# Optimization experiments

Measured on AMD Instinct MI355X. Metric: run time of the kernel, lower is better.

## Reference

```python
import jax, jax.numpy as jnp
import numpy as np

NEG_SLOPE = 0.2  # PyG GATConv default leaky_relu negative_slope
BN_EPS = 1e-5


def gat_layer(x, src, dst, W, a_src, a_dst, bias):
    """PyG-style GATConv (self-loops already appended to src/dst).
    x: [N, F_in], W: [F_in, H*C], a_src/a_dst: [H, C], bias: [H*C].
    Returns [N, H*C] (concat heads)."""
    N = x.shape[0]
    H, C = a_src.shape
    h = (x @ W).reshape(N, H, C)                      # [N, H, C]
    al_src = jnp.sum(h * a_src[None], axis=-1)        # [N, H]
    al_dst = jnp.sum(h * a_dst[None], axis=-1)        # [N, H]
    e = jax.nn.leaky_relu(al_src[src] + al_dst[dst], NEG_SLOPE)  # [E, H]
    # segment softmax over destination neighborhoods
    m = jax.ops.segment_max(e, dst, num_segments=N)   # [N, H]
    ee = jnp.exp(e - m[dst])
    denom = jax.ops.segment_sum(ee, dst, num_segments=N)  # [N, H]
    alpha = ee / denom[dst]                           # [E, H]
    out = jax.ops.segment_sum(alpha[:, :, None] * h[src], dst, num_segments=N)  # [N, H, C]
    return out.reshape(N, H * C) + bias


def batch_norm(x, gamma, beta):
    mu = jnp.mean(x, axis=0)
    var = jnp.var(x, axis=0)  # biased, matches torch BN training stats
    return gamma * (x - mu) * jax.lax.rsqrt(var + BN_EPS) + beta


def setup_inputs() -> dict:
    key = jax.random.key(0)
    N, F, H, C = 50000, 128, 4, 64
    E = 400000
    HC = H * C  # 256
    ks = jax.random.split(key, 24)

    def glorot(k, shape, fan_in):
        return jax.random.normal(k, shape, dtype=jnp.float32) * (1.0 / np.sqrt(fan_in))

    inp = {
        "x": jax.random.normal(ks[0], (N, F), dtype=jnp.float32),
        "edge_index": jax.random.randint(ks[1], (2, E), 0, N, dtype=jnp.int64),
        # conv1: F -> H*C
        "W1": glorot(ks[2], (F, HC), F),
        "a1s": glorot(ks[3], (H, C), C),
        "a1d": glorot(ks[4], (H, C), C),
        "b1": jnp.zeros((HC,), jnp.float32),
        # conv2: H*C -> H*C
        "W2": glorot(ks[5], (HC, HC), HC),
        "a2s": glorot(ks[6], (H, C), C),
        "a2d": glorot(ks[7], (H, C), C),
        "b2": jnp.zeros((HC,), jnp.float32),
        # conv3: H*C -> C (1 head)
        "W3": glorot(ks[8], (HC, C), HC),
        "a3s": glorot(ks[9], (1, C), C),
        "a3d": glorot(ks[10], (1, C), C),
        "b3": jnp.zeros((C,), jnp.float32),
        # batch norms
        "g1": jnp.ones((HC,), jnp.float32),
        "be1": jnp.zeros((HC,), jnp.float32),
        "g2": jnp.ones((HC,), jnp.float32),
        "be2": jnp.zeros((HC,), jnp.float32),
        # MLP head: C -> C//2 -> 2
        "fw1": glorot(ks[11], (C, C // 2), C),
        "fb1": jnp.zeros((C // 2,), jnp.float32),
        "fw2": glorot(ks[12], (C // 2, 2), C // 2),
        "fb2": jnp.zeros((2,), jnp.float32),
    }
    return inp


def reference(x, edge_index, W1, a1s, a1d, b1, W2, a2s, a2d, b2,
              W3, a3s, a3d, b3, g1, be1, g2, be2, fw1, fb1, fw2, fb2):
    N = x.shape[0]
    loop = jnp.arange(N, dtype=edge_index.dtype)
    src = jnp.concatenate([edge_index[0], loop])  # self-loops (PyG default)
    dst = jnp.concatenate([edge_index[1], loop])

    h = gat_layer(x, src, dst, W1, a1s, a1d, b1)
    h = jax.nn.elu(batch_norm(h, g1, be1))
    h = gat_layer(h, src, dst, W2, a2s, a2d, b2)
    h = jax.nn.elu(batch_norm(h, g2, be2))
    h = jax.nn.elu(gat_layer(h, src, dst, W3, a3s, a3d, b3))
    h = jax.nn.relu(h @ fw1 + fb1)
    return h @ fw2 + fb2  # [N, 2] logits
```

## Files before the change

### kernel.cpp

```cpp
#include <hip/hip_runtime.h>
#include <math.h>
#include <stdint.h>

typedef __attribute__((ext_vector_type(8))) short short8v;
typedef __attribute__((ext_vector_type(4))) float float4v;

__device__ __forceinline__ float bf2f(unsigned short u) {
  return __uint_as_float((unsigned int)u << 16);
}
__device__ __forceinline__ unsigned short f2bf(float f) {
  unsigned int u = __float_as_uint(f);
  unsigned int r = (u + 0x7FFFu + ((u >> 16) & 1u)) >> 16;
  return (unsigned short)r;
}
__device__ __forceinline__ float exp_lrelu(float x) {
  x = x > 0.f ? x : 0.2f * x;
  return expf(x);
}

typedef __attribute__((address_space(3))) void lds_void;
typedef const __attribute__((address_space(1))) void glb_void;
__device__ __forceinline__ void gload_lds16(const void* g, void* l) {
  __builtin_amdgcn_global_load_lds((glb_void*)g, (lds_void*)l, 16, 0, 0);
}

__global__ void wprep_kernel(const float* __restrict__ W, unsigned short* __restrict__ Wh,
                             int K, int Nw)
{
  int t = blockIdx.x * 256 + threadIdx.x;
  if (t >= K * Nw) return;
  int i = t & 7;
  int lane = (t >> 3) & 63;
  int frag = t >> 9;
  int ktiles = K >> 5;
  int n_tile = frag / ktiles, k_tile = frag - n_tile * ktiles;
  int k = k_tile * 32 + ((lane >> 4) << 3) + i;
  int n = (n_tile << 4) + (lane & 15);
  Wh[t] = f2bf(W[(size_t)k * Nw + n]);
}

__global__ __launch_bounds__(256) void split_kernel(const float* __restrict__ in,
    unsigned short* __restrict__ hi, size_t n4)
{
  size_t i0 = (size_t)blockIdx.x * 256 + threadIdx.x;
  size_t stride = (size_t)gridDim.x * 256;
  for (size_t idx = i0; idx < n4; idx += stride) {
    float4 v = ((const float4*)in)[idx];
    ushort4 h;
    h.x = f2bf(v.x); h.y = f2bf(v.y); h.z = f2bf(v.z); h.w = f2bf(v.w);
    ((ushort4*)hi)[idx] = h;
  }
}

__global__ __launch_bounds__(256) void bnsplit_kernel(const unsigned short* __restrict__ act,
    const float* __restrict__ scale, const float* __restrict__ shift,
    unsigned short* __restrict__ hi, size_t nchunks)
{
  size_t i0 = (size_t)blockIdx.x * 256 + threadIdx.x;
  size_t stride = (size_t)gridDim.x * 256;
  for (size_t idx = i0; idx < nchunks; idx += stride) {
    ushort4 u = ((const ushort4*)act)[idx];
    int f = (int)((idx * 4) & 255);
    float4 sc = *(const float4*)(scale + f);
    float4 sh = *(const float4*)(shift + f);
    float v0 = fmaf(bf2f(u.x), sc.x, sh.x);
    float v1 = fmaf(bf2f(u.y), sc.y, sh.y);
    float v2 = fmaf(bf2f(u.z), sc.z, sh.z);
    float v3 = fmaf(bf2f(u.w), sc.w, sh.w);
    v0 = v0 > 0.f ? v0 : expm1f(v0);
    v1 = v1 > 0.f ? v1 : expm1f(v1);
    v2 = v2 > 0.f ? v2 : expm1f(v2);
    v3 = v3 > 0.f ? v3 : expm1f(v3);
    ushort4 h;
    h.x = f2bf(v0); h.y = f2bf(v1); h.z = f2bf(v2); h.w = f2bf(v3);
    ((ushort4*)hi)[idx] = h;
  }
}

template<int MI, int WM, int WN, int KSTEPS, int HEADS>
__global__ __launch_bounds__(256) void gemm_al(
    const unsigned short* __restrict__ Ah, const unsigned short* __restrict__ Bh,
    const float* __restrict__ a_s, const float* __restrict__ a_d,
    unsigned short* __restrict__ C, float* __restrict__ al_s, float* __restrict__ al_d,
    int M)
{
  constexpr int BM = WM * MI * 16;
  constexpr int NG = BM / 64;
  constexpr int TILEB = NG * 8192;
  constexpr int Nw = WN * 64, K = KSTEPS * 64;
  constexpr int KT32 = KSTEPS * 2;
  __shared__ __align__(16) unsigned char smem[2][TILEB];

  const int wid = threadIdx.x >> 6, lane = threadIdx.x & 63;
  const int wm = wid / WN, wn = wid % WN;
  const int m0 = blockIdx.x * BM;
  const int n0 = wn * 64;
  const int ar = lane & 15;
  const int cchunk = lane >> 4;
  const int ntile0 = n0 >> 4;

  float4v acc[MI][4];
#pragma unroll
  for (int mi = 0; mi < MI; ++mi)
#pragma unroll
    for (int ni = 0; ni < 4; ++ni)
      acc[mi][ni] = (float4v){0.f, 0.f, 0.f, 0.f};

  auto stage = [&](int buf, int ks) {
#pragma unroll
    for (int j = wid; j < NG * 8; j += 4) {
      int g = j >> 3, c = j & 7;
      const unsigned short* gp = Ah + (size_t)(m0 + g * 64 + lane) * K + ks * 64 + c * 8;
      gload_lds16(gp, &smem[buf][g * 8192 + c * 1024 + lane * 16]);
    }
  };

  stage(0, 0);
  int cur = 0;
  for (int ks = 0; ks < KSTEPS; ++ks) {
    __syncthreads();
    short8v bh[2][4];
#pragma unroll
    for (int hh = 0; hh < 2; ++hh)
#pragma unroll
      for (int ni = 0; ni < 4; ++ni) {
        int kt = ks * 2 + hh;
        size_t off = (((size_t)(ntile0 + ni) * KT32 + kt) * 64 + lane) * 8;
        bh[hh][ni] = *(const short8v*)(Bh + off);
      }
    if (ks + 1 < KSTEPS) stage(cur ^ 1, ks + 1);
    short8v ah[2][MI];
#pragma unroll
    for (int hh = 0; hh < 2; ++hh)
#pragma unroll
      for (int mi = 0; mi < MI; ++mi) {
        int row = wm * MI * 16 + mi * 16 + ar;
        int c = hh * 4 + cchunk;
        int off = (row >> 6) * 8192 + c * 1024 + (row & 63) * 16;
        ah[hh][mi] = *(const short8v*)&smem[cur][off];
      }
#pragma unroll
    for (int hh = 0; hh < 2; ++hh)
#pragma unroll
      for (int mi = 0; mi < MI; ++mi)
#pragma unroll
        for (int ni = 0; ni < 4; ++ni)
          acc[mi][ni] = __builtin_amdgcn_mfma_f32_16x16x32_bf16(ah[hh][mi], bh[hh][ni], acc[mi][ni], 0, 0, 0);
    cur ^= 1;
  }

  const int cc = lane & 15;
#pragma unroll
  for (int mi = 0; mi < MI; ++mi) {
    int rowb = m0 + wm * MI * 16 + mi * 16 + ((lane >> 4) << 2);
#pragma unroll
    for (int r = 0; r < 4; ++r) {
      int row = rowb + r;
      if (row < M) {
#pragma unroll
        for (int ni = 0; ni < 4; ++ni)
          C[(size_t)row * Nw + n0 + ni * 16 + cc] = f2bf(acc[mi][ni][r]);
      }
    }
  }

  const int head = (HEADS == 4) ? wn : 0;
  float as_[4], ad_[4];
#pragma unroll
  for (int ni = 0; ni < 4; ++ni) {
    as_[ni] = a_s[head * 64 + ni * 16 + cc];
    ad_[ni] = a_d[head * 64 + ni * 16 + cc];
  }
#pragma unroll
  for (int mi = 0; mi < MI; ++mi) {
#pragma unroll
    for (int r = 0; r < 4; ++r) {
      float h0 = bf2f(f2bf(acc[mi][0][r]));
      float h1 = bf2f(f2bf(acc[mi][1][r]));
      float h2 = bf2f(f2bf(acc[mi][2][r]));
      float h3 = bf2f(f2bf(acc[mi][3][r]));
      float ps = h0 * as_[0] + h1 * as_[1] + h2 * as_[2] + h3 * as_[3];
      float pd = h0 * ad_[0] + h1 * ad_[1] + h2 * ad_[2] + h3 * ad_[3];
#pragma unroll
      for (int off = 1; off < 16; off <<= 1) {
        ps += __shfl_xor(ps, off);
        pd += __shfl_xor(pd, off);
      }
      int row = m0 + wm * MI * 16 + mi * 16 + ((lane >> 4) << 2) + r;
      if (cc == 0 && row < M) {
        al_s[row * HEADS + head] = ps;
        al_d[row * HEADS + head] = pd;
      }
    }
  }
}

__global__ void count_kernel(const int* __restrict__ dst, int E, int Etot, int* __restrict__ counts)
{
  int e = blockIdx.x * 256 + threadIdx.x;
  if (e >= Etot) return;
  int d = (e < E) ? dst[e] : (e - E);
  atomicAdd(&counts[d], 1);
}

__global__ void block_sum_kernel(const int* __restrict__ counts, int N, int* __restrict__ bsums)
{
  __shared__ int sd[256];
  int i = blockIdx.x * 256 + threadIdx.x;
  sd[threadIdx.x] = (i < N) ? counts[i] : 0;
  __syncthreads();
  for (int off = 128; off; off >>= 1) {
    if (threadIdx.x < off) sd[threadIdx.x] += sd[threadIdx.x + off];
    __syncthreads();
  }
  if (threadIdx.x == 0) bsums[blockIdx.x] = sd[0];
}

__global__ void scan_bsums_kernel(int* bsums, int nb)
{
  __shared__ int sd[256];
  int t = threadIdx.x;
  int v = (t < nb) ? bsums[t] : 0;
  sd[t] = v;
  __syncthreads();
  for (int off = 1; off < 256; off <<= 1) {
    int x = (t >= off) ? sd[t - off] : 0;
    __syncthreads();
    sd[t] += x;
    __syncthreads();
  }
  if (t < nb) bsums[t] = sd[t] - v;
}

__global__ void scan_write_kernel(const int* __restrict__ counts, int N,
                                  const int* __restrict__ bsums, int* __restrict__ rowStart, int Etot)
{
  __shared__ int sd[256];
  int i = blockIdx.x * 256 + threadIdx.x;
  int v = (i < N) ? counts[i] : 0;
  sd[threadIdx.x] = v;
  __syncthreads();
  for (int off = 1; off < 256; off <<= 1) {
    int x = (threadIdx.x >= off) ? sd[threadIdx.x - off] : 0;
    __syncthreads();
    sd[threadIdx.x] += x;
    __syncthreads();
  }
  if (i < N) rowStart[i] = bsums[blockIdx.x] + sd[threadIdx.x] - v;
  if (i == N - 1) rowStart[N] = Etot;
}

__global__ void fill_kernel(const int* __restrict__ src, const int* __restrict__ dst,
                            int E, int Etot, const int* __restrict__ rowStart,
                            int* __restrict__ cursor, int* __restrict__ csrSrc)
{
  int e = blockIdx.x * 256 + threadIdx.x;
  if (e >= Etot) return;
  int s, d;
  if (e < E) { s = src[e]; d = dst[e]; } else { s = d = e - E; }
  int pos = rowStart[d] + atomicAdd(&cursor[d], 1);
  csrSrc[pos] = s;
}

template<int HC_, bool OUT16>
__global__ __launch_bounds__(256) void aggregate_fused(
    const unsigned short* __restrict__ h16,
    const float* __restrict__ als, const float* __restrict__ ald,
    const int* __restrict__ csrSrc, const int* __restrict__ rowStart,
    void* __restrict__ outp, int N, const float* __restrict__ bias, int doElu)
{
  constexpr int H_ = HC_ / 64;
  constexpr int FPL = HC_ / 64;
  __shared__ float ldsW[4][64 * H_];
  const int wl = threadIdx.x >> 6;
  int wid = blockIdx.x * 4 + wl;
  if (wid >= N) return;
  const int lane = threadIdx.x & 63;
  const int head = (H_ == 4) ? (lane >> 4) : 0;
  const int start = rowStart[wid], end = rowStart[wid + 1];

  float ad0, ad1, ad2, ad3;
  if (H_ == 4) {
    float4 adv = ((const float4*)ald)[wid];
    ad0 = adv.x; ad1 = adv.y; ad2 = adv.z; ad3 = adv.w;
  } else {
    ad0 = ald[wid]; ad1 = ad2 = ad3 = 0.f;
  }

  float acc[FPL] = {};
  float wsum = 0.f;

  for (int base = start; base < end; base += 64) {
    int cnt = end - base; if (cnt > 64) cnt = 64;
    int s_l = 0;
    if (lane < cnt) {
      s_l = csrSrc[base + lane];
      if (H_ == 4) {
        float4 av = ((const float4*)als)[s_l];
        float4 w4;
        w4.x = exp_lrelu(av.x + ad0);
        w4.y = exp_lrelu(av.y + ad1);
        w4.z = exp_lrelu(av.z + ad2);
        w4.w = exp_lrelu(av.w + ad3);
        *(float4*)&ldsW[wl][lane * 4] = w4;
      } else {
        ldsW[wl][lane] = exp_lrelu(als[s_l] + ad0);
      }
    }
    int i = 0;
    for (; i + 4 <= cnt; i += 4) {
      int s0 = __shfl(s_l, i);
      int s1 = __shfl(s_l, i + 1);
      int s2 = __shfl(s_l, i + 2);
      int s3 = __shfl(s_l, i + 3);
      float w0 = ldsW[wl][(i + 0) * H_ + head];
      float w1 = ldsW[wl][(i + 1) * H_ + head];
      float w2 = ldsW[wl][(i + 2) * H_ + head];
      float w3 = ldsW[wl][(i + 3) * H_ + head];
      if (FPL == 4) {
        ushort4 r0 = ((const ushort4*)(h16 + (size_t)s0 * HC_))[lane];
        ushort4 r1 = ((const ushort4*)(h16 + (size_t)s1 * HC_))[lane];
        ushort4 r2 = ((const ushort4*)(h16 + (size_t)s2 * HC_))[lane];
        ushort4 r3 = ((const ushort4*)(h16 + (size_t)s3 * HC_))[lane];
        wsum += (w0 + w1) + (w2 + w3);
        acc[0] = fmaf(w0, bf2f(r0.x), acc[0]);
        acc[1] = fmaf(w0, bf2f(r0.y), acc[1]);
        acc[2] = fmaf(w0, bf2f(r0.z), acc[2]);
        acc[3] = fmaf(w0, bf2f(r0.w), acc[3]);
        acc[0] = fmaf(w1, bf2f(r1.x), acc[0]);
        acc[1] = fmaf(w1, bf2f(r1.y), acc[1]);
        acc[2] = fmaf(w1, bf2f(r1.z), acc[2]);
        acc[3] = fmaf(w1, bf2f(r1.w), acc[3]);
        acc[0] = fmaf(w2, bf2f(r2.x), acc[0]);
        acc[1] = fmaf(w2, bf2f(r2.y), acc[1]);
        acc[2] = fmaf(w2, bf2f(r2.z), acc[2]);
        acc[3] = fmaf(w2, bf2f(r2.w), acc[3]);
        acc[0] = fmaf(w3, bf2f(r3.x), acc[0]);
        acc[1] = fmaf(w3, bf2f(r3.y), acc[1]);
        acc[2] = fmaf(w3, bf2f(r3.z), acc[2]);
        acc[3] = fmaf(w3, bf2f(r3.w), acc[3]);
      } else {
        unsigned short r0 = h16[(size_t)s0 * HC_ + lane];
        unsigned short r1 = h16[(size_t)s1 * HC_ + lane];
        unsigned short r2 = h16[(size_t)s2 * HC_ + lane];
        unsigned short r3 = h16[(size_t)s3 * HC_ + lane];
        wsum += (w0 + w1) + (w2 + w3);
        acc[0] = fmaf(w0, bf2f(r0), acc[0]);
        acc[0] = fmaf(w1, bf2f(r1), acc[0]);
        acc[0] = fmaf(w2, bf2f(r2), acc[0]);
        acc[0] = fmaf(w3, bf2f(r3), acc[0]);
      }
    }
    for (; i < cnt; ++i) {
      int s0 = __shfl(s_l, i);
      float w0 = ldsW[wl][i * H_ + head];
      wsum += w0;
      if (FPL == 4) {
        ushort4 r0 = ((const ushort4*)(h16 + (size_t)s0 * HC_))[lane];
        acc[0] = fmaf(w0, bf2f(r0.x), acc[0]);
        acc[1] = fmaf(w0, bf2f(r0.y), acc[1]);
        acc[2] = fmaf(w0, bf2f(r0.z), acc[2]);
        acc[3] = fmaf(w0, bf2f(r0.w), acc[3]);
      } else {
        unsigned short r0 = h16[(size_t)s0 * HC_ + lane];
        acc[0] = fmaf(w0, bf2f(r0), acc[0]);
      }
    }
  }

  float inv = 1.0f / wsum;
  if (FPL == 4) {
    float o0 = acc[0] * inv, o1 = acc[1] * inv, o2 = acc[2] * inv, o3 = acc[3] * inv;
    if (bias) {
      const float4 b = ((const float4*)bias)[lane];
      o0 += b.x; o1 += b.y; o2 += b.z; o3 += b.w;
    }
    if (doElu) {
      o0 = o0 > 0.f ? o0 : expm1f(o0);
      o1 = o1 > 0.f ? o1 : expm1f(o1);
      o2 = o2 > 0.f ? o2 : expm1f(o2);
      o3 = o3 > 0.f ? o3 : expm1f(o3);
    }
    if (OUT16) {
      ushort4 o;
      o.x = f2bf(o0); o.y = f2bf(o1); o.z = f2bf(o2); o.w = f2bf(o3);
      ((ushort4*)((unsigned short*)outp + (size_t)wid * HC_))[lane] = o;
    } else {
      ((float4*)((float*)outp + (size_t)wid * HC_))[lane] = make_float4(o0, o1, o2, o3);
    }
  } else {
    float o = acc[0] * inv;
    if (bias) o += bias[lane];
    if (doElu) o = o > 0.f ? o : expm1f(o);
    if (OUT16) ((unsigned short*)outp)[(size_t)wid * HC_ + lane] = f2bf(o);
    else       ((float*)outp)[(size_t)wid * HC_ + lane] = o;
  }
}

__global__ __launch_bounds__(256) void bn_stats_kernel(const unsigned short* __restrict__ x, int N,
                                float* __restrict__ partials)
{
  const int wid = threadIdx.x >> 6, lane = threadIdx.x & 63;
  const int gw = blockIdx.x * 4 + wid;
  const int tw = gridDim.x * 4;
  float4 s = make_float4(0.f, 0.f, 0.f, 0.f);
  float4 q = make_float4(0.f, 0.f, 0.f, 0.f);
#pragma unroll 4
  for (int r = gw; r < N; r += tw) {
    ushort4 u = ((const ushort4*)(x + (size_t)r * 256))[lane];
    float v0 = bf2f(u.x), v1 = bf2f(u.y), v2 = bf2f(u.z), v3 = bf2f(u.w);
    s.x += v0; s.y += v1; s.z += v2; s.w += v3;
    q.x = fmaf(v0, v0, q.x); q.y = fmaf(v1, v1, q.y);
    q.z = fmaf(v2, v2, q.z); q.w = fmaf(v3, v3, q.w);
  }
  __shared__ float ls[4][512];
  *(float4*)&ls[wid][lane * 4] = s;
  *(float4*)&ls[wid][256 + lane * 4] = q;
  __syncthreads();
  const int t = threadIdx.x;
  float a = ls[0][t] + ls[1][t] + ls[2][t] + ls[3][t];
  float b = ls[0][t + 256] + ls[1][t + 256] + ls[2][t + 256] + ls[3][t + 256];
  partials[blockIdx.x * 512 + t] = a;
  partials[blockIdx.x * 512 + 256 + t] = b;
}

__global__ void bn_final_kernel(const float* __restrict__ partials, int nblk,
                                const float* __restrict__ g, const float* __restrict__ be,
                                int N, float* __restrict__ scale, float* __restrict__ shift)
{
  int f = threadIdx.x;
  float s = 0.f, q = 0.f;
#pragma unroll 8
  for (int b = 0; b < nblk; ++b) {
    s += partials[b * 512 + f];
    q += partials[b * 512 + 256 + f];
  }
  float mu = s / N;
  float var = q / N - mu * mu;
  float rs = rsqrtf(var + 1e-5f);
  float sc = g[f] * rs;
  scale[f] = sc;
  shift[f] = be[f] - mu * sc;
}

__global__ __launch_bounds__(256) void mlp_kernel(const float* __restrict__ h,
                           const float* __restrict__ fw1,
                           const float* __restrict__ fb1, const float* __restrict__ fw2,
                           const float* __restrict__ fb2, float* __restrict__ out, int N)
{
  __shared__ float w1s[64][32];
  __shared__ float w2s[32][2];
  __shared__ float b1s[32];
  const int t = threadIdx.x;
  for (int i = t; i < 64 * 32; i += 256) w1s[i >> 5][i & 31] = fw1[i];
  if (t < 64) w2s[t >> 1][t & 1] = fw2[t];
  if (t < 32) b1s[t] = fb1[t];
  __syncthreads();

  int n = blockIdx.x * 256 + t;
  if (n >= N) return;

  float hv[64];
#pragma unroll
  for (int k4 = 0; k4 < 16; ++k4) {
    float4 v = *(const float4*)(h + (size_t)n * 64 + k4 * 4);
    hv[k4 * 4 + 0] = v.x; hv[k4 * 4 + 1] = v.y;
    hv[k4 * 4 + 2] = v.z; hv[k4 * 4 + 3] = v.w;
  }
  float hid[32];
#pragma unroll
  for (int j = 0; j < 32; ++j) hid[j] = b1s[j];
#pragma unroll
  for (int k = 0; k < 64; ++k) {
    float hk = hv[k];
#pragma unroll
    for (int jb = 0; jb < 8; ++jb) {
      float4 wv = *(const float4*)&w1s[k][jb * 4];
      hid[jb * 4 + 0] = fmaf(hk, wv.x, hid[jb * 4 + 0]);
      hid[jb * 4 + 1] = fmaf(hk, wv.y, hid[jb * 4 + 1]);
      hid[jb * 4 + 2] = fmaf(hk, wv.z, hid[jb * 4 + 2]);
      hid[jb * 4 + 3] = fmaf(hk, wv.w, hid[jb * 4 + 3]);
    }
  }
  float p0 = fb2[0], p1 = fb2[1];
#pragma unroll
  for (int j = 0; j < 32; ++j) {
    float r = fmaxf(hid[j], 0.f);
    p0 = fmaf(r, w2s[j][0], p0);
    p1 = fmaf(r, w2s[j][1], p1);
  }
  *(float2*)(out + (size_t)n * 2) = make_float2(p0, p1);
}

extern "C" void kernel_launch(void* const* d_in, const int* in_sizes, int n_in,
                              void* d_out, int out_size, void* d_ws, size_t ws_size,
                              hipStream_t stream)
{
  const float* x   = (const float*)d_in[0];
  const int*   ei  = (const int*)d_in[1];
  const float* W1  = (const float*)d_in[2];
  const float* a1s = (const float*)d_in[3];
  const float* a1d = (const float*)d_in[4];
  const float* W2  = (const float*)d_in[6];
  const float* a2s = (const float*)d_in[7];
  const float* a2d = (const float*)d_in[8];
  const float* W3  = (const float*)d_in[10];
  const float* a3s = (const float*)d_in[11];
  const float* a3d = (const float*)d_in[12];
  const float* b3  = (const float*)d_in[13];
  const float* g1  = (const float*)d_in[14];
  const float* be1 = (const float*)d_in[15];
  const float* g2  = (const float*)d_in[16];
  const float* be2 = (const float*)d_in[17];
  const float* fw1 = (const float*)d_in[18];
  const float* fb1 = (const float*)d_in[19];
  const float* fw2 = (const float*)d_in[20];
  const float* fb2 = (const float*)d_in[21];
  float* out = (float*)d_out;

  const int F = 128;
  const int N = in_sizes[0] / F;
  const int E = in_sizes[1] / 2;
  const int Etot = E + N;
  const int* srcIdx = ei;
  const int* dstIdx = ei + E;

  char* w = (char*)d_ws;
  auto alloc = [&](size_t bytes) -> void* {
    void* p = (void*)w;
    w += (bytes + 255) & ~(size_t)255;
    return p;
  };
  unsigned short* h16  = (unsigned short*)alloc((size_t)N * 256 * 2);
  unsigned short* act16= (unsigned short*)alloc((size_t)N * 256 * 2);
  float* actf    = (float*)alloc((size_t)N * 64 * 4);
  unsigned short* aBf  = (unsigned short*)alloc((size_t)N * 256 * 2);
  float* als     = (float*)alloc((size_t)N * 4 * 4);
  float* ald     = (float*)alloc((size_t)N * 4 * 4);
  int*   counts  = (int*)alloc((size_t)N * 4);
  int*   cursor  = (int*)alloc((size_t)N * 4);
  int*   rowStart= (int*)alloc((size_t)(N + 1) * 4);
  int*   csrSrc  = (int*)alloc((size_t)Etot * 4);
  int*   bsums   = (int*)alloc((size_t)((N + 255) / 256) * 4);
  float* partials= (float*)alloc((size_t)128 * 512 * 4);
  float* scale1  = (float*)alloc(256 * 4);
  float* shift1  = (float*)alloc(256 * 4);
  float* scale2  = (float*)alloc(256 * 4);
  float* shift2  = (float*)alloc(256 * 4);
  unsigned short* w1h = (unsigned short*)alloc((size_t)128 * 256 * 2);
  unsigned short* w2h = (unsigned short*)alloc((size_t)256 * 256 * 2);
  unsigned short* w3h = (unsigned short*)alloc((size_t)256 * 64 * 2);
  (void)alloc(65536);

  const int nb = (N + 255) / 256;
  const int ebk = (Etot + 255) / 256;
  const int aggBlocks = (N + 3) / 4;

  wprep_kernel<<<(128 * 256 + 255) / 256, 256, 0, stream>>>(W1, w1h, 128, 256);
  wprep_kernel<<<(256 * 256 + 255) / 256, 256, 0, stream>>>(W2, w2h, 256, 256);
  wprep_kernel<<<(256 * 64 + 255) / 256, 256, 0, stream>>>(W3, w3h, 256, 64);

  hipMemsetAsync(counts, 0, (size_t)N * 4, stream);
  hipMemsetAsync(cursor, 0, (size_t)N * 4, stream);
  count_kernel<<<ebk, 256, 0, stream>>>(dstIdx, E, Etot, counts);
  block_sum_kernel<<<nb, 256, 0, stream>>>(counts, N, bsums);
  scan_bsums_kernel<<<1, 256, 0, stream>>>(bsums, nb);
  scan_write_kernel<<<nb, 256, 0, stream>>>(counts, N, bsums, rowStart, Etot);
  fill_kernel<<<ebk, 256, 0, stream>>>(srcIdx, dstIdx, E, Etot, rowStart, cursor, csrSrc);

  dim3 g12((N + 63) / 64, 1);
  dim3 g3((N + 127) / 128, 1);

  split_kernel<<<2048, 256, 0, stream>>>(x, aBf, (size_t)N * 128 / 4);
  gemm_al<4, 1, 4, 2, 4><<<g12, 256, 0, stream>>>(aBf, w1h, a1s, a1d, h16, als, ald, N);
  aggregate_fused<256, true><<<aggBlocks, 256, 0, stream>>>(h16, als, ald, csrSrc, rowStart, act16, N, nullptr, 0);
  bn_stats_kernel<<<128, 256, 0, stream>>>(act16, N, partials);
  bn_final_kernel<<<1, 256, 0, stream>>>(partials, 128, g1, be1, N, scale1, shift1);

  bnsplit_kernel<<<2048, 256, 0, stream>>>(act16, scale1, shift1, aBf, (size_t)N * 64);
  gemm_al<4, 1, 4, 4, 4><<<g12, 256, 0, stream>>>(aBf, w2h, a2s, a2d, h16, als, ald, N);
  aggregate_fused<256, true><<<aggBlocks, 256, 0, stream>>>(h16, als, ald, csrSrc, rowStart, act16, N, nullptr, 0);
  bn_stats_kernel<<<128, 256, 0, stream>>>(act16, N, partials);
  bn_final_kernel<<<1, 256, 0, stream>>>(partials, 128, g2, be2, N, scale2, shift2);

  bnsplit_kernel<<<2048, 256, 0, stream>>>(act16, scale2, shift2, aBf, (size_t)N * 64);
  gemm_al<2, 4, 1, 4, 1><<<g3, 256, 0, stream>>>(aBf, w3h, a3s, a3d, h16, als, ald, N);
  aggregate_fused<64, false><<<aggBlocks, 256, 0, stream>>>(h16, als, ald, csrSrc, rowStart, actf, N, b3, 1);

  mlp_kernel<<<(N + 255) / 256, 256, 0, stream>>>(actf, fw1, fb1, fw2, fb2, out, N);
}
```

Baseline: 306.5 us.

## Split GEMM across 2D grid with 128-thread blocks, merge weight prep and memsets

The attention-fused GEMM now uses 128-thread blocks and a second grid dimension over column groups, so each block handles a 64-row tile and half the heads (or a smaller tile for the single-head layer). This roughly doubles the number of blocks and halves LDS per block, aiming for better occupancy and load balance. The A tile is then staged once per column-group block, so A traffic through L2 doubles. The three weight-conversion launches are merged into one kernel, and the two counter memsets into one contiguous memset, to cut launch overhead.

```diff
diff --git a/kernel.cpp b/kernel.cpp
--- a/kernel.cpp
+++ b/kernel.cpp
@@ -24,11 +24,9 @@
   __builtin_amdgcn_global_load_lds((glb_void*)g, (lds_void*)l, 16, 0, 0);
 }
 
-__global__ void wprep_kernel(const float* __restrict__ W, unsigned short* __restrict__ Wh,
-                             int K, int Nw)
-{
-  int t = blockIdx.x * 256 + threadIdx.x;
-  if (t >= K * Nw) return;
+__device__ __forceinline__ void wprep_one(const float* W, unsigned short* Wh,
+                                          int t, int K, int Nw)
+{
   int i = t & 7;
   int lane = (t >> 3) & 63;
   int frag = t >> 9;
@@ -37,6 +35,19 @@
   int k = k_tile * 32 + ((lane >> 4) << 3) + i;
   int n = (n_tile << 4) + (lane & 15);
   Wh[t] = f2bf(W[(size_t)k * Nw + n]);
+}
+
+__global__ void wprep_all_kernel(const float* __restrict__ W1, unsigned short* __restrict__ w1h,
+                                 const float* __restrict__ W2, unsigned short* __restrict__ w2h,
+                                 const float* __restrict__ W3, unsigned short* __restrict__ w3h)
+{
+  int t = blockIdx.x * 256 + threadIdx.x;
+  const int s1 = 128 * 256, s2 = 256 * 256, s3 = 256 * 64;
+  if (t < s1) { wprep_one(W1, w1h, t, 128, 256); return; }
+  t -= s1;
+  if (t < s2) { wprep_one(W2, w2h, t, 256, 256); return; }
+  t -= s2;
+  if (t < s3) { wprep_one(W3, w3h, t, 256, 64); }
 }
 
 __global__ __launch_bounds__(256) void split_kernel(const float* __restrict__ in,
@@ -78,23 +89,25 @@
 }
 
 template<int MI, int WM, int WN, int KSTEPS, int HEADS>
-__global__ __launch_bounds__(256) void gemm_al(
+__global__ __launch_bounds__(128) void gemm_al(
     const unsigned short* __restrict__ Ah, const unsigned short* __restrict__ Bh,
     const float* __restrict__ a_s, const float* __restrict__ a_d,
     unsigned short* __restrict__ C, float* __restrict__ al_s, float* __restrict__ al_d,
     int M)
 {
+  constexpr int NWAVES = WM * WN;
   constexpr int BM = WM * MI * 16;
-  constexpr int NG = BM / 64;
-  constexpr int TILEB = NG * 8192;
-  constexpr int Nw = WN * 64, K = KSTEPS * 64;
+  constexpr int TILEB = BM * 64 * 2;
+  constexpr int Nw = HEADS * 64;
+  constexpr int K = KSTEPS * 64;
   constexpr int KT32 = KSTEPS * 2;
   __shared__ __align__(16) unsigned char smem[2][TILEB];
 
   const int wid = threadIdx.x >> 6, lane = threadIdx.x & 63;
   const int wm = wid / WN, wn = wid % WN;
+  const int gn = blockIdx.y * WN + wn;
   const int m0 = blockIdx.x * BM;
-  const int n0 = wn * 64;
+  const int n0 = gn * 64;
   const int ar = lane & 15;
   const int cchunk = lane >> 4;
   const int ntile0 = n0 >> 4;
@@ -108,10 +121,9 @@
 
   auto stage = [&](int buf, int ks) {
 #pragma unroll
-    for (int j = wid; j < NG * 8; j += 4) {
-      int g = j >> 3, c = j & 7;
-      const unsigned short* gp = Ah + (size_t)(m0 + g * 64 + lane) * K + ks * 64 + c * 8;
-      gload_lds16(gp, &smem[buf][g * 8192 + c * 1024 + lane * 16]);
+    for (int c = wid; c < 8; c += NWAVES) {
+      const unsigned short* gp = Ah + (size_t)(m0 + lane) * K + ks * 64 + c * 8;
+      gload_lds16(gp, &smem[buf][c * 1024 + lane * 16]);
     }
   };
 
@@ -136,7 +148,7 @@
       for (int mi = 0; mi < MI; ++mi) {
         int row = wm * MI * 16 + mi * 16 + ar;
         int c = hh * 4 + cchunk;
-        int off = (row >> 6) * 8192 + c * 1024 + (row & 63) * 16;
+        int off = c * 1024 + row * 16;
         ah[hh][mi] = *(const short8v*)&smem[cur][off];
       }
 #pragma unroll
@@ -164,7 +176,7 @@
     }
   }
 
-  const int head = (HEADS == 4) ? wn : 0;
+  const int head = (HEADS == 4) ? gn : 0;
   float as_[4], ad_[4];
 #pragma unroll
   for (int ni = 0; ni < 4; ++ni) {
@@ -537,6 +549,7 @@
   unsigned short* aBf  = (unsigned short*)alloc((size_t)N * 256 * 2);
   float* als     = (float*)alloc((size_t)N * 4 * 4);
   float* ald     = (float*)alloc((size_t)N * 4 * 4);
+  const size_t cntPad = ((size_t)N * 4 + 255) & ~(size_t)255;
   int*   counts  = (int*)alloc((size_t)N * 4);
   int*   cursor  = (int*)alloc((size_t)N * 4);
   int*   rowStart= (int*)alloc((size_t)(N + 1) * 4);
@@ -556,35 +569,33 @@
   const int ebk = (Etot + 255) / 256;
   const int aggBlocks = (N + 3) / 4;
 
-  wprep_kernel<<<(128 * 256 + 255) / 256, 256, 0, stream>>>(W1, w1h, 128, 256);
-  wprep_kernel<<<(256 * 256 + 255) / 256, 256, 0, stream>>>(W2, w2h, 256, 256);
-  wprep_kernel<<<(256 * 64 + 255) / 256, 256, 0, stream>>>(W3, w3h, 256, 64);
-
-  hipMemsetAsync(counts, 0, (size_t)N * 4, stream);
-  hipMemsetAsync(cursor, 0, (size_t)N * 4, stream);
+  const int wtot = 128 * 256 + 256 * 256 + 256 * 64;
+  wprep_all_kernel<<<(wtot + 255) / 256, 256, 0, stream>>>(W1, w1h, W2, w2h, W3, w3h);
+
+  hipMemsetAsync(counts, 0, cntPad + (size_t)N * 4, stream);
   count_kernel<<<ebk, 256, 0, stream>>>(dstIdx, E, Etot, counts);
   block_sum_kernel<<<nb, 256, 0, stream>>>(counts, N, bsums);
   scan_bsums_kernel<<<1, 256, 0, stream>>>(bsums, nb);
   scan_write_kernel<<<nb, 256, 0, stream>>>(counts, N, bsums, rowStart, Etot);
   fill_kernel<<<ebk, 256, 0, stream>>>(srcIdx, dstIdx, E, Etot, rowStart, cursor, csrSrc);
 
-  dim3 g12((N + 63) / 64, 1);
-  dim3 g3((N + 127) / 128, 1);
+  dim3 g12((N + 63) / 64, 2);
+  dim3 g3((N + 63) / 64, 1);
 
   split_kernel<<<2048, 256, 0, stream>>>(x, aBf, (size_t)N * 128 / 4);
-  gemm_al<4, 1, 4, 2, 4><<<g12, 256, 0, stream>>>(aBf, w1h, a1s, a1d, h16, als, ald, N);
+  gemm_al<4, 1, 2, 2, 4><<<g12, 128, 0, stream>>>(aBf, w1h, a1s, a1d, h16, als, ald, N);
   aggregate_fused<256, true><<<aggBlocks, 256, 0, stream>>>(h16, als, ald, csrSrc, rowStart, act16, N, nullptr, 0);
   bn_stats_kernel<<<128, 256, 0, stream>>>(act16, N, partials);
   bn_final_kernel<<<1, 256, 0, stream>>>(partials, 128, g1, be1, N, scale1, shift1);
 
   bnsplit_kernel<<<2048, 256, 0, stream>>>(act16, scale1, shift1, aBf, (size_t)N * 64);
-  gemm_al<4, 1, 4, 4, 4><<<g12, 256, 0, stream>>>(aBf, w2h, a2s, a2d, h16, als, ald, N);
+  gemm_al<4, 1, 2, 4, 4><<<g12, 128, 0, stream>>>(aBf, w2h, a2s, a2d, h16, als, ald, N);
   aggregate_fused<256, true><<<aggBlocks, 256, 0, stream>>>(h16, als, ald, csrSrc, rowStart, act16, N, nullptr, 0);
   bn_stats_kernel<<<128, 256, 0, stream>>>(act16, N, partials);
   bn_final_kernel<<<1, 256, 0, stream>>>(partials, 128, g2, be2, N, scale2, shift2);
 
   bnsplit_kernel<<<2048, 256, 0, stream>>>(act16, scale2, shift2, aBf, (size_t)N * 64);
-  gemm_al<2, 4, 1, 4, 1><<<g3, 256, 0, stream>>>(aBf, w3h, a3s, a3d, h16, als, ald, N);
+  gemm_al<2, 2, 1, 4, 1><<<g3, 128, 0, stream>>>(aBf, w3h, a3s, a3d, h16, als, ald, N);
   aggregate_fused<64, false><<<aggBlocks, 256, 0, stream>>>(h16, als, ald, csrSrc, rowStart, actf, N, b3, 1);
 
   mlp_kernel<<<(N + 255) / 256, 256, 0, stream>>>(actf, fw1, fb1, fw2, fb2, out, N);
```

Result: no change. 306.1 us (-0.1%).
